# Kernel tuning notes

Hardware: AMD Instinct MI355X
Metric: run time of the kernel (lower is better)

Reference implementation:

```python
import jax, jax.numpy as jnp
import numpy as np

N_PATTERNS = 8192  # N: number of stored patterns (rows of Weights)
N_BITS = 4096      # n: pattern dimension (state length)


def setup_inputs() -> dict:
    key = jax.random.key(0)
    k1, k2, k3 = jax.random.split(key, 3)
    # Stored patterns (Weights) and initial state are +/-1 spins, as in a
    # discrete Hopfield / dense associative memory.
    weights = jnp.where(jax.random.normal(k1, (N_PATTERNS, N_BITS)) >= 0, 1.0, -1.0).astype(jnp.float32)
    state = jnp.where(jax.random.normal(k2, (N_BITS,)) >= 0, 1.0, -1.0).astype(jnp.float32)
    # Shuffled visit order (original uses random.shuffle on arange(n)).
    perm = jax.random.permutation(k3, N_BITS).astype(jnp.int32)
    return {"weights": weights, "state": state, "perm": perm}


def _energy_from_h(h):
    # energy(state) = -sum(F(W @ state, 2)) with F(x,2) = relu(x)**2
    return -jnp.sum(jnp.square(jnp.maximum(h, 0.0)))


def reference(weights, state, perm):
    # h = W @ state, maintained incrementally: flipping bit i changes h by
    # -2 * state[i] * W[:, i], which is exactly the same linear math as the
    # original full recompute per flip.
    h0 = weights @ state                      # [N]
    e0 = _energy_from_h(h0)

    def step(carry, i):
        h, vals, prev = carry
        col = jnp.take(weights, i, axis=1)    # W[:, i], gather of one column
        vi = vals[i]
        h_new = h - 2.0 * vi * col
        e_new = _energy_from_h(h_new)
        accept = e_new < prev                 # accept flip iff energy decreases
        h = jnp.where(accept, h_new, h)
        vals = vals.at[i].set(jnp.where(accept, -vi, vi))
        prev = jnp.where(accept, e_new, prev)
        return (h, vals, prev), None

    (_, vals, _), _ = jax.lax.scan(step, (h0, state, e0), perm)
    return vals
```

## Files before the change

### kernel.cpp

```cpp
#include <hip/hip_runtime.h>
#include <cstdint>

#define NPAT 8192
#define NBITS 4096

typedef float f32x2 __attribute__((ext_vector_type(2)));
typedef unsigned int u32;


__global__ void pack_kernel(const float* __restrict__ W, const float* __restrict__ state,
                            uint32_t* __restrict__ Bt) {
    int b = blockIdx.x & 63;
    int i = (blockIdx.x >> 6) * 256 + threadIdx.x;
    uint32_t spre = (__float_as_uint(state[i]) >> 31) ^ 1u;
    uint32_t wd0 = 0, wd1 = 0, wd2 = 0, wd3 = 0;
    const float* base = W + (size_t)(128 * b) * NBITS + i;
    #pragma unroll
    for (int q = 0; q < 128; ++q) {
        uint32_t bit = (__float_as_uint(base[(size_t)q * NBITS]) >> 31) ^ spre;
        int j = q & 7, k = q >> 3;
        int a = j >> 1, hi = j & 1;
        uint32_t add = bit << (2 * k + hi);
        if (a == 0) wd0 |= add;
        else if (a == 1) wd1 |= add;
        else if (a == 2) wd2 |= add;
        else wd3 |= add;
    }
    *(uint4*)(Bt + (size_t)i * 256 + 4 * b) = make_uint4(wd0, wd1, wd2, wd3);
}

__global__ void gemv_kernel(const float* __restrict__ W, const float* __restrict__ state,
                            float* __restrict__ h0) {
    int wid = threadIdx.x >> 6, lane = threadIdx.x & 63;
    int p = blockIdx.x * 4 + wid;
    const float* row = W + (size_t)p * NBITS;
    float acc = 0.f;
    for (int k = lane; k < NBITS; k += 64) acc += row[k] * state[k];
    #pragma unroll
    for (int d = 1; d < 64; d <<= 1) acc += __shfl_xor(acc, d, 64);
    if (lane == 0) h0[p] = acc;
}

__device__ __forceinline__ float tree_reduce(float x) {
    x = __uint_as_float(__builtin_amdgcn_update_dpp(__float_as_uint(x), __float_as_uint(x),
                                                    0xB1, 0xf, 0xf, false)) + x;
    x = __uint_as_float(__builtin_amdgcn_update_dpp(__float_as_uint(x), __float_as_uint(x),
                                                    0x4E, 0xf, 0xf, false)) + x;
    x = __uint_as_float(__builtin_amdgcn_update_dpp(__float_as_uint(x), __float_as_uint(x),
                                                    0x141, 0xf, 0xf, false)) + x;
    x = __uint_as_float(__builtin_amdgcn_update_dpp(__float_as_uint(x), __float_as_uint(x),
                                                    0x140, 0xf, 0xf, false)) + x;
#if __has_builtin(__builtin_amdgcn_permlane16_swap)
    {
        auto pr = __builtin_amdgcn_permlane16_swap(__float_as_uint(x), __float_as_uint(x),
                                                   false, false);
        x = __uint_as_float(pr[0]) + __uint_as_float(pr[1]);
    }
#else
    x = __int_as_float(__builtin_amdgcn_ds_swizzle(__float_as_int(x), 0x401F)) + x;
#endif
#if __has_builtin(__builtin_amdgcn_permlane32_swap)
    {
        auto pr = __builtin_amdgcn_permlane32_swap(__float_as_uint(x), __float_as_uint(x),
                                                   false, false);
        x = __uint_as_float(pr[0]) + __uint_as_float(pr[1]);
    }
#else
    x += __shfl_xor(x, 32, 64);
#endif
    return x;
}

__device__ __forceinline__ f32x2 pkmax0(f32x2 v) {
    f32x2 z = {0.0f, 0.0f};
    return __builtin_elementwise_max(v, z);
}

#define GEN_DT(dst, w, tab)                                                   \
    _Pragma("unroll")                                                         \
    for (int k = 0; k < 16; ++k) {                                            \
        u32 _off = (k < 2) ? ((w << (3 - 2 * k)) & 0x18u)                     \
                           : ((w >> (2 * k - 3)) & 0x18u);                    \
        dst[k] = *(const f32x2*)((const char*)(tab) + _off);                  \
    }

__launch_bounds__(256, 1)
__global__ void seq_kernel(const uint32_t* __restrict__ Bt, const float* __restrict__ h0,
                           const float* __restrict__ state, const int* __restrict__ perm,
                           float* __restrict__ out) {
    __shared__ alignas(16) float part[2][4][4];
    __shared__ alignas(8)  f32x2 dtab[4];
    __shared__ int2 pv[NBITS];

    const int t = threadIdx.x;
    const int b = t >> 2, a = t & 3;
    const int lane = t & 63, wid = t >> 6;

    for (int q = t; q < NBITS; q += 256) {
        int ii = perm[q];
        pv[q] = make_int2(ii, __float_as_int(state[ii]));
    }
    if (t < 4) dtab[t] = (f32x2){(t & 1) ? -2.0f : 2.0f, (t & 2) ? -2.0f : 2.0f};

    f32x2 h[16];
    #pragma unroll
    for (int k = 0; k < 16; ++k) h[k] = *(const f32x2*)(h0 + 128 * b + 2 * a + 8 * k);

    __syncthreads();

    u32 wA[4], wB[4];
    #pragma unroll
    for (int r = 0; r < 4; ++r) {
        wA[r] = Bt[(size_t)pv[2 * r].x * 256 + t];
        wB[r] = Bt[(size_t)pv[2 * r + 1].x * 256 + t];
    }

    f32x2 d0[2][16], d1[2][16];
    GEN_DT(d0[0], wA[0], dtab);
    GEN_DT(d1[0], wB[0], dtab);

    float Sprev;
    {
        f32x2 r;
        #pragma unroll
        for (int k = 0; k < 16; ++k) {
            f32x2 x = pkmax0(h[k]);
            r = (k == 0) ? x * x : __builtin_elementwise_fma(x, x, r);
        }
        float red = tree_reduce(r.x + r.y);
        if (lane == 0) part[0][wid][0] = red;
        asm volatile("s_waitcnt lgkmcnt(0)\n\ts_barrier" ::: "memory");
        float4 p0 = *(const float4*)(&part[0][0][0]);
        float4 p1 = *(const float4*)(&part[0][1][0]);
        float4 p2 = *(const float4*)(&part[0][2][0]);
        float4 p3 = *(const float4*)(&part[0][3][0]);
        Sprev = (p0.x + p1.x) + (p2.x + p3.x);
    }

    for (int rb = 0; rb < NBITS / 2; rb += 4) {
        #pragma unroll
        for (int u = 0; u < 4; ++u) {
            const int rr = rb + u;
            const int s  = 2 * rr;
            const int pb = u & 1;
            const int cu = u & 1;

            int4 pvc = *(const int4*)(&pv[s]);

            f32x2 ra, rbv, rc;
            #pragma unroll
            for (int k = 0; k < 16; ++k) {
                f32x2 va = h[k] + d0[cu][k];
                f32x2 vb = h[k] + d1[cu][k];
                f32x2 vc = va + d1[cu][k];
                f32x2 xa = pkmax0(va), xb = pkmax0(vb), xc = pkmax0(vc);
                if (k == 0) { ra = xa * xa; rbv = xb * xb; rc = xc * xc; }
                else {
                    ra  = __builtin_elementwise_fma(xa, xa, ra);
                    rbv = __builtin_elementwise_fma(xb, xb, rbv);
                    rc  = __builtin_elementwise_fma(xc, xc, rc);
                }
            }
            float Ra = tree_reduce(ra.x + ra.y);
            float Rb = tree_reduce(rbv.x + rbv.y);
            float Rc = tree_reduce(rc.x + rc.y);
            if (lane == 0)
                *(float4*)(&part[pb][wid][0]) = make_float4(Ra, Rb, Rc, 0.0f);
            asm volatile("s_waitcnt lgkmcnt(0)\n\ts_barrier" ::: "memory");

            float4 p0 = *(const float4*)(&part[pb][0][0]);
            float4 p1 = *(const float4*)(&part[pb][1][0]);
            float4 p2 = *(const float4*)(&part[pb][2][0]);
            float4 p3 = *(const float4*)(&part[pb][3][0]);

            GEN_DT(d0[cu ^ 1], wA[(u + 1) & 3], dtab);
            GEN_DT(d1[cu ^ 1], wB[(u + 1) & 3], dtab);

            int li = (s + 8 < NBITS) ? s + 8 : NBITS - 2;
            int4 pvn = *(const int4*)(&pv[li]);
            wA[u] = Bt[(size_t)pvn.x * 256 + t];
            wB[u] = Bt[(size_t)pvn.z * 256 + t];

            float Sa = (p0.x + p1.x) + (p2.x + p3.x);
            float Sb = (p0.y + p1.y) + (p2.y + p3.y);
            float Sc = (p0.z + p1.z) + (p2.z + p3.z);
            bool acc0 = Sa > Sprev;
            bool acc1 = acc0 ? (Sc > Sa) : (Sb > Sprev);
            Sprev = acc1 ? (acc0 ? Sc : Sb) : (acc0 ? Sa : Sprev);

            if (t == 0) {
                float v0 = __int_as_float(pvc.y), v1 = __int_as_float(pvc.w);
                out[pvc.x] = acc0 ? -v0 : v0;
                out[pvc.z] = acc1 ? -v1 : v1;
            }

            float f0s = acc0 ? 1.0f : 0.0f, f1s = acc1 ? 1.0f : 0.0f;
            f32x2 f0 = {f0s, f0s}, f1 = {f1s, f1s};
            #pragma unroll
            for (int k = 0; k < 16; ++k) {
                f32x2 hh = __builtin_elementwise_fma(d0[cu][k], f0, h[k]);
                h[k] = __builtin_elementwise_fma(d1[cu][k], f1, hh);
            }
        }
    }
}

extern "C" void kernel_launch(void* const* d_in, const int* in_sizes, int n_in,
                              void* d_out, int out_size, void* d_ws, size_t ws_size,
                              hipStream_t stream) {
    const float* W     = (const float*)d_in[0];
    const float* state = (const float*)d_in[1];
    const int*   perm  = (const int*)d_in[2];
    float*       out   = (float*)d_out;

    uint32_t* Bt = (uint32_t*)d_ws;
    float*    h0 = (float*)((char*)d_ws + (size_t)4096 * 256 * 4);

    pack_kernel<<<1024, 256, 0, stream>>>(W, state, Bt);
    gemv_kernel<<<2048, 256, 0, stream>>>(W, state, h0);
    seq_kernel<<<1, 256, 0, stream>>>(Bt, h0, state, perm, out);
}
```

Baseline: 2.186 ms.

## Build ±2 deltas from packed bits with bit ops instead of LDS table lookups

Changes the bit packing layout so each 32-bit word holds the low and high halves in separate 16-bit fields. The seq kernel then builds each ±2.0 delta directly with shift, mask and OR, replacing the LDS table gather and the double-buffered delta arrays. The h update now branches uniformly on the accept flags (via readfirstlane) and skips work when nothing is accepted. The prefetch depth drops from 4 to 2, and packed f32x2 math becomes scalar float math, which may cost VALU throughput on the sequential critical path.

```diff
diff --git a/kernel.cpp b/kernel.cpp
--- a/kernel.cpp
+++ b/kernel.cpp
@@ -20,7 +20,7 @@
         uint32_t bit = (__float_as_uint(base[(size_t)q * NBITS]) >> 31) ^ spre;
         int j = q & 7, k = q >> 3;
         int a = j >> 1, hi = j & 1;
-        uint32_t add = bit << (2 * k + hi);
+        uint32_t add = bit << (16 * hi + k);
         if (a == 0) wd0 |= add;
         else if (a == 1) wd1 |= add;
         else if (a == 2) wd2 |= add;
@@ -71,26 +71,15 @@
     return x;
 }
 
-__device__ __forceinline__ f32x2 pkmax0(f32x2 v) {
-    f32x2 z = {0.0f, 0.0f};
-    return __builtin_elementwise_max(v, z);
-}
-
-#define GEN_DT(dst, w, tab)                                                   \
-    _Pragma("unroll")                                                         \
-    for (int k = 0; k < 16; ++k) {                                            \
-        u32 _off = (k < 2) ? ((w << (3 - 2 * k)) & 0x18u)                     \
-                           : ((w >> (2 * k - 3)) & 0x18u);                    \
-        dst[k] = *(const f32x2*)((const char*)(tab) + _off);                  \
-    }
+#define DLO(w, k) __uint_as_float((((w) << (31 - (k))) & 0x80000000u) | 0x40000000u)
+#define DHI(w, k) __uint_as_float((((w) << (15 - (k))) & 0x80000000u) | 0x40000000u)
 
 __launch_bounds__(256, 1)
 __global__ void seq_kernel(const uint32_t* __restrict__ Bt, const float* __restrict__ h0,
                            const float* __restrict__ state, const int* __restrict__ perm,
                            float* __restrict__ out) {
     __shared__ alignas(16) float part[2][4][4];
-    __shared__ alignas(8)  f32x2 dtab[4];
-    __shared__ int2 pv[NBITS];
+    __shared__ alignas(16) int2 pv[NBITS];
 
     const int t = threadIdx.x;
     const int b = t >> 2, a = t & 3;
@@ -100,83 +89,80 @@
         int ii = perm[q];
         pv[q] = make_int2(ii, __float_as_int(state[ii]));
     }
-    if (t < 4) dtab[t] = (f32x2){(t & 1) ? -2.0f : 2.0f, (t & 2) ? -2.0f : 2.0f};
-
-    f32x2 h[16];
+
+    float hl[16], hh[16];
     #pragma unroll
-    for (int k = 0; k < 16; ++k) h[k] = *(const f32x2*)(h0 + 128 * b + 2 * a + 8 * k);
+    for (int k = 0; k < 16; ++k) {
+        f32x2 p2 = *(const f32x2*)(h0 + 128 * b + 2 * a + 8 * k);
+        hl[k] = p2.x; hh[k] = p2.y;
+    }
 
     __syncthreads();
 
-    u32 wA[4], wB[4];
-    #pragma unroll
-    for (int r = 0; r < 4; ++r) {
-        wA[r] = Bt[(size_t)pv[2 * r].x * 256 + t];
-        wB[r] = Bt[(size_t)pv[2 * r + 1].x * 256 + t];
-    }
-
-    f32x2 d0[2][16], d1[2][16];
-    GEN_DT(d0[0], wA[0], dtab);
-    GEN_DT(d1[0], wB[0], dtab);
+    u32 wA[2], wB[2];
+    wA[0] = Bt[(size_t)pv[0].x * 256 + t];
+    wB[0] = Bt[(size_t)pv[1].x * 256 + t];
+    wA[1] = Bt[(size_t)pv[2].x * 256 + t];
+    wB[1] = Bt[(size_t)pv[3].x * 256 + t];
 
     float Sprev;
     {
-        f32x2 r;
+        float ral, rah;
         #pragma unroll
         for (int k = 0; k < 16; ++k) {
-            f32x2 x = pkmax0(h[k]);
-            r = (k == 0) ? x * x : __builtin_elementwise_fma(x, x, r);
+            float xl = fmaxf(hl[k], 0.f), xh = fmaxf(hh[k], 0.f);
+            ral = k ? fmaf(xl, xl, ral) : xl * xl;
+            rah = k ? fmaf(xh, xh, rah) : xh * xh;
         }
-        float red = tree_reduce(r.x + r.y);
-        if (lane == 0) part[0][wid][0] = red;
+        float red = tree_reduce(ral + rah);
+        if (lane == 0) part[1][wid][0] = red;
         asm volatile("s_waitcnt lgkmcnt(0)\n\ts_barrier" ::: "memory");
-        float4 p0 = *(const float4*)(&part[0][0][0]);
-        float4 p1 = *(const float4*)(&part[0][1][0]);
-        float4 p2 = *(const float4*)(&part[0][2][0]);
-        float4 p3 = *(const float4*)(&part[0][3][0]);
-        Sprev = (p0.x + p1.x) + (p2.x + p3.x);
-    }
-
-    for (int rb = 0; rb < NBITS / 2; rb += 4) {
+        Sprev = (part[1][0][0] + part[1][1][0]) + (part[1][2][0] + part[1][3][0]);
+    }
+
+    for (int rb = 0; rb < NBITS / 2; rb += 2) {
         #pragma unroll
-        for (int u = 0; u < 4; ++u) {
+        for (int u = 0; u < 2; ++u) {
             const int rr = rb + u;
             const int s  = 2 * rr;
-            const int pb = u & 1;
-            const int cu = u & 1;
+            const u32 w0 = wA[u], w1 = wB[u];
 
             int4 pvc = *(const int4*)(&pv[s]);
 
-            f32x2 ra, rbv, rc;
+            float ral, rah, rbl, rbh, rcl, rch;
             #pragma unroll
             for (int k = 0; k < 16; ++k) {
-                f32x2 va = h[k] + d0[cu][k];
-                f32x2 vb = h[k] + d1[cu][k];
-                f32x2 vc = va + d1[cu][k];
-                f32x2 xa = pkmax0(va), xb = pkmax0(vb), xc = pkmax0(vc);
-                if (k == 0) { ra = xa * xa; rbv = xb * xb; rc = xc * xc; }
-                else {
-                    ra  = __builtin_elementwise_fma(xa, xa, ra);
-                    rbv = __builtin_elementwise_fma(xb, xb, rbv);
-                    rc  = __builtin_elementwise_fma(xc, xc, rc);
+                float d0l = DLO(w0, k), d0h = DHI(w0, k);
+                float d1l = DLO(w1, k), d1h = DHI(w1, k);
+                float val = hl[k] + d0l, vah = hh[k] + d0h;
+                float vbl = hl[k] + d1l, vbh = hh[k] + d1h;
+                float vcl = val + d1l,  vch = vah + d1h;
+                float xal = fmaxf(val, 0.f), xah = fmaxf(vah, 0.f);
+                float xbl = fmaxf(vbl, 0.f), xbh = fmaxf(vbh, 0.f);
+                float xcl = fmaxf(vcl, 0.f), xch = fmaxf(vch, 0.f);
+                if (k == 0) {
+                    ral = xal * xal; rah = xah * xah;
+                    rbl = xbl * xbl; rbh = xbh * xbh;
+                    rcl = xcl * xcl; rch = xch * xch;
+                } else {
+                    ral = fmaf(xal, xal, ral); rah = fmaf(xah, xah, rah);
+                    rbl = fmaf(xbl, xbl, rbl); rbh = fmaf(xbh, xbh, rbh);
+                    rcl = fmaf(xcl, xcl, rcl); rch = fmaf(xch, xch, rch);
                 }
             }
-            float Ra = tree_reduce(ra.x + ra.y);
-            float Rb = tree_reduce(rbv.x + rbv.y);
-            float Rc = tree_reduce(rc.x + rc.y);
+            float Ra = tree_reduce(ral + rah);
+            float Rb = tree_reduce(rbl + rbh);
+            float Rc = tree_reduce(rcl + rch);
             if (lane == 0)
-                *(float4*)(&part[pb][wid][0]) = make_float4(Ra, Rb, Rc, 0.0f);
+                *(float4*)(&part[u][wid][0]) = make_float4(Ra, Rb, Rc, 0.0f);
             asm volatile("s_waitcnt lgkmcnt(0)\n\ts_barrier" ::: "memory");
 
-            float4 p0 = *(const float4*)(&part[pb][0][0]);
-            float4 p1 = *(const float4*)(&part[pb][1][0]);
-            float4 p2 = *(const float4*)(&part[pb][2][0]);
-            float4 p3 = *(const float4*)(&part[pb][3][0]);
-
-            GEN_DT(d0[cu ^ 1], wA[(u + 1) & 3], dtab);
-            GEN_DT(d1[cu ^ 1], wB[(u + 1) & 3], dtab);
-
-            int li = (s + 8 < NBITS) ? s + 8 : NBITS - 2;
+            float4 p0 = *(const float4*)(&part[u][0][0]);
+            float4 p1 = *(const float4*)(&part[u][1][0]);
+            float4 p2 = *(const float4*)(&part[u][2][0]);
+            float4 p3 = *(const float4*)(&part[u][3][0]);
+
+            int li = (s + 4 < NBITS) ? s + 4 : NBITS - 2;
             int4 pvn = *(const int4*)(&pv[li]);
             wA[u] = Bt[(size_t)pvn.x * 256 + t];
             wB[u] = Bt[(size_t)pvn.z * 256 + t];
@@ -184,6 +170,7 @@
             float Sa = (p0.x + p1.x) + (p2.x + p3.x);
             float Sb = (p0.y + p1.y) + (p2.y + p3.y);
             float Sc = (p0.z + p1.z) + (p2.z + p3.z);
+
             bool acc0 = Sa > Sprev;
             bool acc1 = acc0 ? (Sc > Sa) : (Sb > Sprev);
             Sprev = acc1 ? (acc0 ? Sc : Sb) : (acc0 ? Sa : Sprev);
@@ -194,12 +181,28 @@
                 out[pvc.z] = acc1 ? -v1 : v1;
             }
 
-            float f0s = acc0 ? 1.0f : 0.0f, f1s = acc1 ? 1.0f : 0.0f;
-            f32x2 f0 = {f0s, f0s}, f1 = {f1s, f1s};
-            #pragma unroll
-            for (int k = 0; k < 16; ++k) {
-                f32x2 hh = __builtin_elementwise_fma(d0[cu][k], f0, h[k]);
-                h[k] = __builtin_elementwise_fma(d1[cu][k], f1, hh);
+            int a0 = __builtin_amdgcn_readfirstlane(acc0 ? 1 : 0);
+            int a1 = __builtin_amdgcn_readfirstlane(acc1 ? 1 : 0);
+            if (a0) {
+                if (a1) {
+                    #pragma unroll
+                    for (int k = 0; k < 16; ++k) {
+                        hl[k] = (hl[k] + DLO(w0, k)) + DLO(w1, k);
+                        hh[k] = (hh[k] + DHI(w0, k)) + DHI(w1, k);
+                    }
+                } else {
+                    #pragma unroll
+                    for (int k = 0; k < 16; ++k) {
+                        hl[k] = hl[k] + DLO(w0, k);
+                        hh[k] = hh[k] + DHI(w0, k);
+                    }
+                }
+            } else if (a1) {
+                #pragma unroll
+                for (int k = 0; k < 16; ++k) {
+                    hl[k] = hl[k] + DLO(w1, k);
+                    hh[k] = hh[k] + DHI(w1, k);
+                }
             }
         }
     }
```

Result: slower. 2.759 ms (+26.2%).
